# Optimization experiments

Measured on AMD Instinct MI355X. Metric: run time of the kernel, lower is better.

The kernel has to match this reference:

```python
import jax, jax.numpy as jnp
import numpy as np

N = 100000   # nodes
E = 1600000  # edges
G = 64       # graphs in batch
DIMS = [(7, 128), (128, 128), (128, 256)]
EPS = 1e-5


def setup_inputs() -> dict:
    key = jax.random.key(0)
    ks = jax.random.split(key, 32)
    inp = {}
    inp["x"] = jax.random.normal(ks[0], (N, 7), dtype=jnp.float32)
    inp["edge_index"] = jax.random.randint(ks[1], (2, E), 0, N, dtype=jnp.int64)
    inp["batch"] = jnp.sort(jax.random.randint(ks[2], (N,), 0, G, dtype=jnp.int64))
    ki = 3
    for i, (din, dout) in enumerate(DIMS):
        inp[f"Wl{i}"] = jax.random.normal(ks[ki], (din, dout), dtype=jnp.float32) * 0.05; ki += 1
        inp[f"bl{i}"] = jnp.zeros((dout,), dtype=jnp.float32)
        inp[f"Wr{i}"] = jax.random.normal(ks[ki], (din, dout), dtype=jnp.float32) * 0.05; ki += 1
        inp[f"g{i}"] = jax.random.uniform(ks[ki], (dout,), dtype=jnp.float32) + 0.5; ki += 1
        inp[f"be{i}"] = jax.random.normal(ks[ki], (dout,), dtype=jnp.float32) * 0.1; ki += 1
        inp[f"rm{i}"] = jax.random.normal(ks[ki], (dout,), dtype=jnp.float32) * 0.1; ki += 1
        inp[f"rv{i}"] = jax.random.uniform(ks[ki], (dout,), dtype=jnp.float32) + 0.5; ki += 1
    return inp


def _sage(x, src, dst, Wl, bl, Wr):
    # mean-aggregate neighbor features: out[i] = mean_{(j->i)} x[j]
    agg = jax.ops.segment_sum(x[src], dst, num_segments=N)          # [N, din]
    cnt = jax.ops.segment_sum(jnp.ones((src.shape[0],), x.dtype), dst, num_segments=N)
    mean = agg / jnp.maximum(cnt, 1.0)[:, None]
    return x @ Wl + bl + mean @ Wr


def _bn_relu(x, g, be, rm, rv):
    # BatchNorm1d in eval mode (running stats) + ReLU; dropout is a no-op in eval
    return jax.nn.relu((x - rm) * jax.lax.rsqrt(rv + EPS) * g + be)


def reference(x, edge_index, batch,
              Wl0, bl0, Wr0, g0, be0, rm0, rv0,
              Wl1, bl1, Wr1, g1, be1, rm1, rv1,
              Wl2, bl2, Wr2, g2, be2, rm2, rv2):
    src, dst = edge_index[0], edge_index[1]
    layers = [(Wl0, bl0, Wr0, g0, be0, rm0, rv0),
              (Wl1, bl1, Wr1, g1, be1, rm1, rv1),
              (Wl2, bl2, Wr2, g2, be2, rm2, rv2)]
    for Wl, bl, Wr, g, be, rm, rv in layers:
        x = _sage(x, src, dst, Wl, bl, Wr)
        x = _bn_relu(x, g, be, rm, rv)
    pooled = jax.ops.segment_sum(x, batch, num_segments=G)  # global_add_pool
    return (pooled, x)
```

## Files before the change

### kernel.cpp

```cpp
#include <hip/hip_runtime.h>
#include <hip/hip_bf16.h>

#define EPSV 1e-5f
#define PSHIFT 6
#define PMASK 63
#define BCAP 256
#define BSHIFT 8
#define XG 8

typedef __attribute__((ext_vector_type(8))) short bf16x8;
typedef __attribute__((ext_vector_type(4))) float f32x4;

__device__ __forceinline__ float bf2f(unsigned short u) {
    unsigned x = ((unsigned)u) << 16;
    return __builtin_bit_cast(float, x);
}
__device__ __forceinline__ unsigned short f2bf(float f) {
    unsigned x = __builtin_bit_cast(unsigned, f);
    unsigned r = (x + 0x7fffu + ((x >> 16) & 1u)) >> 16;
    return (unsigned short)r;
}

__global__ __launch_bounds__(256) void k_bucket(const int* __restrict__ src,
                                                const int* __restrict__ dst,
                                                int* __restrict__ bcnt,
                                                unsigned* __restrict__ staging,
                                                int E, int NPART) {
    int i = blockIdx.x * 256 + threadIdx.x;
    if (i >= E) return;
    int g = blockIdx.x & (XG - 1);
    int d = __builtin_nontemporal_load(&dst[i]);
    int s = __builtin_nontemporal_load(&src[i]);
    int p = d >> PSHIFT;
    int b = g * NPART + p;
    int slot = atomicAdd(&bcnt[b], 1);
    if (slot < BCAP)
        staging[((size_t)b << BSHIFT) + slot] = ((unsigned)s << PSHIFT) | (unsigned)(d & PMASK);
}

__global__ __launch_bounds__(256) void k_meta(const int* __restrict__ bcnt,
                                              int* __restrict__ pbase,
                                              int* __restrict__ off,
                                              const int* __restrict__ batch,
                                              int* __restrict__ gstart,
                                              int NPART, int Nn, int G) {
    if (blockIdx.x == 1) {
        int g = threadIdx.x;
        if (g > G) return;
        if (g == G) {
            gstart[G] = Nn;
            return;
        }
        int lo = 0, hi = Nn;
        while (lo < hi) {
            int mid = (lo + hi) >> 1;
            if (batch[mid] < g) lo = mid + 1;
            else hi = mid;
        }
        gstart[g] = lo;
        return;
    }
    __shared__ int red[256];
    int t = threadIdx.x;
    int chunk = (NPART + 255) / 256;
    int lo = t * chunk, hi = min(lo + chunk, NPART);
    int s = 0;
    for (int p = lo; p < hi; p++) {
        int tt = 0;
#pragma unroll
        for (int g = 0; g < XG; g++) tt += min(bcnt[g * NPART + p], BCAP);
        pbase[p] = tt;
        s += tt;
    }
    red[t] = s;
    __syncthreads();
    for (int d = 1; d < 256; d <<= 1) {
        int v = (t >= d) ? red[t - d] : 0;
        __syncthreads();
        red[t] += v;
        __syncthreads();
    }
    int base = (t == 0) ? 0 : red[t - 1];
    for (int p = lo; p < hi; p++) {
        int tt = pbase[p];
        pbase[p] = base;
        base += tt;
    }
    if (t == 255) off[Nn] = red[255];
}

__global__ __launch_bounds__(256) void k_build(const int* __restrict__ bcnt,
                                               const unsigned* __restrict__ staging,
                                               const int* __restrict__ pbase,
                                               int* __restrict__ off,
                                               int* __restrict__ csr,
                                               int NPART, int Nn) {
    __shared__ unsigned ed[XG * BCAP];
    __shared__ int srt[XG * BCAP];
    __shared__ int cnt[64], loff[64], cur[64];
    __shared__ int sb[XG + 1];
    int p = blockIdx.x, t = threadIdx.x;
    if (t < 64) cnt[t] = 0;
    if (t == 0) {
        int acc = 0;
#pragma unroll
        for (int g = 0; g < XG; g++) {
            sb[g] = acc;
            acc += min(bcnt[g * NPART + p], BCAP);
        }
        sb[XG] = acc;
    }
    __syncthreads();
    int tot = sb[XG];
#pragma unroll
    for (int g = 0; g < XG; g++) {
        int c = sb[g + 1] - sb[g];
        const unsigned* sp = staging + (((size_t)(g * NPART + p)) << BSHIFT);
        for (int j = t; j < c; j += 256) ed[sb[g] + j] = __builtin_nontemporal_load(&sp[j]);
    }
    __syncthreads();
    for (int j = t; j < tot; j += 256) atomicAdd(&cnt[ed[j] & PMASK], 1);
    __syncthreads();
    if (t == 0) {
        int a = 0;
        for (int j = 0; j < 64; j++) {
            loff[j] = a;
            cur[j] = a;
            a += cnt[j];
        }
    }
    __syncthreads();
    int base = pbase[p];
    int node0 = p << PSHIFT;
    if (t < 64 && node0 + t < Nn) off[node0 + t] = base + loff[t];
    for (int j = t; j < tot; j += 256) {
        unsigned e = ed[j];
        int pos = atomicAdd(&cur[e & PMASK], 1);
        srt[pos] = (int)(e >> PSHIFT);
    }
    __syncthreads();
    for (int j = t; j < tot; j += 256) csr[base + j] = srt[j];
}


__global__ __launch_bounds__(256) void k_agg7(const float* __restrict__ x,
                                              const int* __restrict__ off,
                                              const int* __restrict__ csr,
                                              float* __restrict__ mean, int n) {
    int i = (blockIdx.x * 256 + threadIdx.x) >> 3;
    int r = threadIdx.x & 7;
    if (i >= n) return;
    int a = off[i], b = off[i + 1];
    float acc = 0.f;
    if (r < 7) {
        int j = a;
        for (; j + 1 < b; j += 2)
            acc += x[(size_t)csr[j] * 7 + r] + x[(size_t)csr[j + 1] * 7 + r];
        if (j < b) acc += x[(size_t)csr[j] * 7 + r];
    }
    float inv = 1.0f / (float)max(b - a, 1);
    if (r < 7) mean[(size_t)i * 7 + r] = acc * inv;
}

__global__ __launch_bounds__(256) void k_agg128(const unsigned short* __restrict__ x,
                                                const int* __restrict__ off,
                                                const int* __restrict__ csr,
                                                unsigned short* __restrict__ mean,
                                                int n) {
    int h = (blockIdx.x * 256 + threadIdx.x) >> 5;
    int sl = threadIdx.x & 31;
    if (h >= n) return;
    int a = off[h], b = off[h + 1];
    float a0 = 0.f, a1 = 0.f, a2 = 0.f, a3 = 0.f;
    int j = a;
    for (; j + 3 < b; j += 4) {
        int s0 = csr[j], s1 = csr[j + 1], s2 = csr[j + 2], s3 = csr[j + 3];
        ushort4 v0 = *(const ushort4*)&x[(size_t)s0 * 128 + sl * 4];
        ushort4 v1 = *(const ushort4*)&x[(size_t)s1 * 128 + sl * 4];
        ushort4 v2 = *(const ushort4*)&x[(size_t)s2 * 128 + sl * 4];
        ushort4 v3 = *(const ushort4*)&x[(size_t)s3 * 128 + sl * 4];
        a0 += bf2f(v0.x) + bf2f(v1.x) + bf2f(v2.x) + bf2f(v3.x);
        a1 += bf2f(v0.y) + bf2f(v1.y) + bf2f(v2.y) + bf2f(v3.y);
        a2 += bf2f(v0.z) + bf2f(v1.z) + bf2f(v2.z) + bf2f(v3.z);
        a3 += bf2f(v0.w) + bf2f(v1.w) + bf2f(v2.w) + bf2f(v3.w);
    }
    for (; j < b; j++) {
        ushort4 v = *(const ushort4*)&x[(size_t)csr[j] * 128 + sl * 4];
        a0 += bf2f(v.x);
        a1 += bf2f(v.y);
        a2 += bf2f(v.z);
        a3 += bf2f(v.w);
    }
    float inv = 1.0f / (float)max(b - a, 1);
    ushort4 o;
    o.x = f2bf(a0 * inv);
    o.y = f2bf(a1 * inv);
    o.z = f2bf(a2 * inv);
    o.w = f2bf(a3 * inv);
    *(ushort4*)&mean[(size_t)h * 128 + sl * 4] = o;
}


__global__ __launch_bounds__(256) void k_prepw_all(
    const float* __restrict__ Wl1, const float* __restrict__ Wr1,
    const float* __restrict__ Wl2, const float* __restrict__ Wr2,
    unsigned short* __restrict__ Wlt1, unsigned short* __restrict__ Wrt1,
    unsigned short* __restrict__ Wlt2, unsigned short* __restrict__ Wrt2) {
    int u = blockIdx.x * 256 + threadIdx.x;
    const float* W;
    unsigned short* Wt;
    int Ncols, v;
    if (u < 32768) {
        v = u & 16383;
        W = (u < 16384) ? Wl1 : Wr1;
        Wt = (u < 16384) ? Wlt1 : Wrt1;
        Ncols = 128;
    } else {
        v = (u - 32768) & 32767;
        W = (u < 65536) ? Wl2 : Wr2;
        Wt = (u < 65536) ? Wlt2 : Wrt2;
        Ncols = 256;
    }
    int n = v % Ncols, k = v / Ncols;
    Wt[(size_t)n * 128 + k] = f2bf(W[(size_t)k * Ncols + n]);
}


__global__ __launch_bounds__(256) void k_layer0(
    const float* __restrict__ x, const float* __restrict__ mean,
    const float* __restrict__ Wl, const float* __restrict__ bl,
    const float* __restrict__ Wr, const float* __restrict__ g,
    const float* __restrict__ be, const float* __restrict__ rm,
    const float* __restrict__ rv, unsigned short* __restrict__ out, int n) {
    int tid = threadIdx.x;
    int col = tid & 127;
    int r = tid >> 7;
    int row = blockIdx.x * 2 + r;
    if (row >= n) return;
    float sc = g[col] * rsqrtf(rv[col] + EPSV);
    float sh = (bl[col] - rm[col]) * sc + be[col];
    const float* xp = x + (size_t)row * 7;
    const float* mp = mean + (size_t)row * 7;
    float acc = 0.f;
#pragma unroll
    for (int k = 0; k < 7; k++) acc += xp[k] * Wl[k * 128 + col];
#pragma unroll
    for (int k = 0; k < 7; k++) acc += mp[k] * Wr[k * 128 + col];
    float h = acc * sc + sh;
    out[(size_t)row * 128 + col] = f2bf(fmaxf(h, 0.f));
}


template <int COLS, int DOUT, bool BF16OUT>
__global__ __launch_bounds__(256) void k_mfma_layer(
    const unsigned short* __restrict__ xin, const unsigned short* __restrict__ meanb,
    const unsigned short* __restrict__ Wlt, const unsigned short* __restrict__ Wrt,
    const float* __restrict__ bl, const float* __restrict__ g,
    const float* __restrict__ be, const float* __restrict__ rm,
    const float* __restrict__ rv, void* __restrict__ outv, int n) {
    __shared__ unsigned short As[64 * 40];
    __shared__ unsigned short Bs[COLS * 40];

    int tid = threadIdx.x;
    int wave = tid >> 6;
    int lane = tid & 63;
    int m = lane & 15;
    int half = lane >> 4;
    int row0 = blockIdx.x * 64;
    int colbase = blockIdx.y * COLS;

    const int NCB = COLS / 16;
    f32x4 acc[NCB] = {};

    for (int s = 0; s < 8; s++) {
        int pass = s >> 2;
        int k0 = (s & 3) * 32;
        const unsigned short* Asrc = pass ? meanb : xin;
        const unsigned short* Wt = pass ? Wrt : Wlt;

        __syncthreads();
        {
            int rr = tid >> 2;
            int ks = (tid & 3) * 8;
            int grow = row0 + rr;
            float4 v = make_float4(0.f, 0.f, 0.f, 0.f);
            if (grow < n) v = *(const float4*)&Asrc[(size_t)grow * 128 + k0 + ks];
            *(float4*)&As[rr * 40 + ks] = v;
        }
#pragma unroll
        for (int rep = 0; rep < COLS / 64; rep++) {
            int u = tid + rep * 256;
            int nn = u >> 2;
            int ks = (u & 3) * 8;
            float4 v = *(const float4*)&Wt[(size_t)(colbase + nn) * 128 + k0 + ks];
            *(float4*)&Bs[nn * 40 + ks] = v;
        }
        __syncthreads();

        bf16x8 a = *(const bf16x8*)&As[(wave * 16 + m) * 40 + half * 8];
#pragma unroll
        for (int cb = 0; cb < NCB; cb++) {
            bf16x8 b = *(const bf16x8*)&Bs[(cb * 16 + m) * 40 + half * 8];
            acc[cb] = __builtin_amdgcn_mfma_f32_16x16x32_bf16(a, b, acc[cb], 0, 0, 0);
        }
    }

    float* outf = (float*)outv;
    unsigned short* outb = (unsigned short*)outv;
#pragma unroll
    for (int cb = 0; cb < NCB; cb++) {
        int col = colbase + cb * 16 + m;
        float sc = g[col] * rsqrtf(rv[col] + EPSV);
        float sh = (bl[col] - rm[col]) * sc + be[col];
#pragma unroll
        for (int reg = 0; reg < 4; reg++) {
            int r0 = row0 + wave * 16 + half * 4 + reg;
            if (r0 < n) {
                float h = fmaxf(acc[cb][reg] * sc + sh, 0.f);
                if (BF16OUT) outb[(size_t)r0 * DOUT + col] = f2bf(h);
                else outf[(size_t)r0 * DOUT + col] = h;
            }
        }
    }
}


__global__ __launch_bounds__(256) void k_pool(const float* __restrict__ x3,
                                              const int* __restrict__ gstart,
                                              float* __restrict__ pooled, int G) {
    const int S = 16;
    int g = blockIdx.x / S;
    int s = blockIdx.x % S;
    int a = gstart[g], b = gstart[g + 1];
    int col = threadIdx.x;
    float acc = 0.f;
    for (int r = a + s; r < b; r += S) acc += x3[(size_t)r * 256 + col];
    atomicAdd(&pooled[g * 256 + col], acc);
}


extern "C" void kernel_launch(void* const* d_in, const int* in_sizes, int n_in,
                              void* d_out, int out_size, void* d_ws, size_t ws_size,
                              hipStream_t stream) {
    const float* x = (const float*)d_in[0];
    const int* ei = (const int*)d_in[1];
    const int* batch = (const int*)d_in[2];
    const int N = in_sizes[0] / 7;
    const int E = in_sizes[1] / 2;
    const int G = 64;
    const int* src = ei;
    const int* dst = ei + E;
    const int NPART = (N + PMASK) >> PSHIFT;

    const float* P[21];
    for (int i = 0; i < 21; i++) P[i] = (const float*)d_in[3 + i];
    const float **L0 = P, **L1 = P + 7, **L2 = P + 14;

    char* w = (char*)d_ws;
    auto carve = [&](size_t bytes) {
        void* p = (void*)w;
        w += (bytes + 255) & ~(size_t)255;
        return p;
    };
    int* bcnt = (int*)carve((size_t)XG * NPART * 4);
    unsigned* staging = (unsigned*)carve((size_t)XG * NPART * BCAP * 4);
    int* pbase = (int*)carve((size_t)NPART * 4);
    int* off = (int*)carve(((size_t)N + 1) * 4);
    int* csr = (int*)carve((size_t)E * 4);
    int* gstart = (int*)carve(((size_t)G + 1) * 4);
    float* mean7 = (float*)carve((size_t)N * 7 * 4);
    unsigned short* x1 = (unsigned short*)carve((size_t)N * 128 * 2);
    unsigned short* meanb = (unsigned short*)carve((size_t)N * 128 * 2);
    unsigned short* Wlt1 = (unsigned short*)carve((size_t)128 * 128 * 2);
    unsigned short* Wrt1 = (unsigned short*)carve((size_t)128 * 128 * 2);
    unsigned short* Wlt2 = (unsigned short*)carve((size_t)128 * 256 * 2);
    unsigned short* Wrt2 = (unsigned short*)carve((size_t)128 * 256 * 2);

    float* pooled = (float*)d_out;
    float* x3 = (float*)d_out + (size_t)G * 256;

    hipMemsetAsync(bcnt, 0, (size_t)XG * NPART * 4, stream);
    hipMemsetAsync(pooled, 0, (size_t)G * 256 * 4, stream);

    k_bucket<<<(E + 255) / 256, 256, 0, stream>>>(src, dst, bcnt, staging, E, NPART);
    k_meta<<<2, 256, 0, stream>>>(bcnt, pbase, off, batch, gstart, NPART, N, G);
    k_build<<<NPART, 256, 0, stream>>>(bcnt, staging, pbase, off, csr, NPART, N);
    k_prepw_all<<<(98304 + 255) / 256, 256, 0, stream>>>(L1[0], L1[2], L2[0], L2[2],
                                                         Wlt1, Wrt1, Wlt2, Wrt2);

    k_agg7<<<(N * 8 + 255) / 256, 256, 0, stream>>>(x, off, csr, mean7, N);
    k_layer0<<<(N + 1) / 2, 256, 0, stream>>>(x, mean7, L0[0], L0[1], L0[2], L0[3],
                                              L0[4], L0[5], L0[6], x1, N);

    k_agg128<<<(N + 7) / 8, 256, 0, stream>>>(x1, off, csr, meanb, N);
    k_mfma_layer<128, 128, true><<<dim3((N + 63) / 64, 1), 256, 0, stream>>>(
        x1, meanb, Wlt1, Wrt1, L1[1], L1[3], L1[4], L1[5], L1[6], x1, N);

    k_agg128<<<(N + 7) / 8, 256, 0, stream>>>(x1, off, csr, meanb, N);
    k_mfma_layer<128, 256, false><<<dim3((N + 63) / 64, 2), 256, 0, stream>>>(
        x1, meanb, Wlt2, Wrt2, L2[1], L2[3], L2[4], L2[5], L2[6], x3, N);

    k_pool<<<G * 16, 256, 0, stream>>>(x3, gstart, pooled, G);
}
```

Baseline: 525.2 us.

## Replace single-pass edge bucketing with two-level block-aggregated radix scatter

The CSR construction used to do one global atomic per edge into XG-replicated 64-node buckets. It is replaced by a two-pass radix scatter. The first pass builds a block-local shared-memory histogram over 2048-node coarse buckets and needs one global atomic per bucket per block. The second pass redistributes each coarse bucket into 64-node partitions with the same block-aggregation trick. The aim is to cut global atomic contention and scattered writes. In exchange it adds an extra pass over the edges, and the CSR array now aliases the first-stage staging buffer.

```diff
diff --git a/kernel.cpp b/kernel.cpp
--- a/kernel.cpp
+++ b/kernel.cpp
@@ -4,9 +4,11 @@
 #define EPSV 1e-5f
 #define PSHIFT 6
 #define PMASK 63
-#define BCAP 256
-#define BSHIFT 8
-#define XG 8
+#define PCAP 1536
+#define B1SHIFT 11
+#define B1MASK ((1 << B1SHIFT) - 1)
+#define B1CAP 34816
+#define SPLIT 16
 
 typedef __attribute__((ext_vector_type(8))) short bf16x8;
 typedef __attribute__((ext_vector_type(4))) float f32x4;
@@ -21,24 +23,75 @@
     return (unsigned short)r;
 }
 
-__global__ __launch_bounds__(256) void k_bucket(const int* __restrict__ src,
-                                                const int* __restrict__ dst,
-                                                int* __restrict__ bcnt,
-                                                unsigned* __restrict__ staging,
-                                                int E, int NPART) {
-    int i = blockIdx.x * 256 + threadIdx.x;
-    if (i >= E) return;
-    int g = blockIdx.x & (XG - 1);
-    int d = __builtin_nontemporal_load(&dst[i]);
-    int s = __builtin_nontemporal_load(&src[i]);
-    int p = d >> PSHIFT;
-    int b = g * NPART + p;
-    int slot = atomicAdd(&bcnt[b], 1);
-    if (slot < BCAP)
-        staging[((size_t)b << BSHIFT) + slot] = ((unsigned)s << PSHIFT) | (unsigned)(d & PMASK);
-}
-
-__global__ __launch_bounds__(256) void k_meta(const int* __restrict__ bcnt,
+
+__global__ __launch_bounds__(256) void k_scatter1(const int* __restrict__ src,
+                                                  const int* __restrict__ dst,
+                                                  int* __restrict__ bcnt1,
+                                                  unsigned* __restrict__ stg1,
+                                                  int E, int NB1) {
+    __shared__ int hist[64], sbase[64], scur[64];
+    int t = threadIdx.x;
+    int base = blockIdx.x * 2048;
+    if (t < 64) { hist[t] = 0; scur[t] = 0; }
+    __syncthreads();
+    unsigned val[8];
+    int cb[8];
+#pragma unroll
+    for (int k = 0; k < 8; k++) {
+        int i = base + k * 256 + t;
+        if (i < E) {
+            int d = __builtin_nontemporal_load(&dst[i]);
+            int s = __builtin_nontemporal_load(&src[i]);
+            cb[k] = d >> B1SHIFT;
+            val[k] = ((unsigned)s << B1SHIFT) | (unsigned)(d & B1MASK);
+            atomicAdd(&hist[cb[k]], 1);
+        } else
+            cb[k] = -1;
+    }
+    __syncthreads();
+    if (t < NB1 && hist[t] > 0) sbase[t] = atomicAdd(&bcnt1[t], hist[t]);
+    __syncthreads();
+#pragma unroll
+    for (int k = 0; k < 8; k++) {
+        if (cb[k] >= 0) {
+            int r = atomicAdd(&scur[cb[k]], 1);
+            int slot = sbase[cb[k]] + r;
+            if (slot < B1CAP) stg1[(size_t)cb[k] * B1CAP + slot] = val[k];
+        }
+    }
+}
+
+__global__ __launch_bounds__(256) void k_scatter2(const int* __restrict__ bcnt1,
+                                                  const unsigned* __restrict__ stg1,
+                                                  int* __restrict__ pcnt,
+                                                  unsigned* __restrict__ pstg) {
+    __shared__ int hist[32], sbase[32], scur[32];
+    int cb = blockIdx.x >> 4;
+    int sl = blockIdx.x & (SPLIT - 1);
+    int t = threadIdx.x;
+    if (t < 32) { hist[t] = 0; scur[t] = 0; }
+    int cnt = min(bcnt1[cb], B1CAP);
+    int per = (cnt + SPLIT - 1) / SPLIT;
+    int lo = sl * per, hi = min(lo + per, cnt);
+    __syncthreads();
+    const unsigned* sp = stg1 + (size_t)cb * B1CAP;
+    for (int j = lo + t; j < hi; j += 256)
+        atomicAdd(&hist[(sp[j] >> 6) & 31], 1);
+    __syncthreads();
+    if (t < 32 && hist[t] > 0) sbase[t] = atomicAdd(&pcnt[(cb << 5) + t], hist[t]);
+    __syncthreads();
+    for (int j = lo + t; j < hi; j += 256) {
+        unsigned v = sp[j];
+        int pr = (v >> 6) & 31;
+        int r = atomicAdd(&scur[pr], 1);
+        int slot = sbase[pr] + r;
+        if (slot < PCAP)
+            pstg[(size_t)((cb << 5) + pr) * PCAP + slot] =
+                ((v >> 5) & ~63u) | (v & 63u);
+    }
+}
+
+__global__ __launch_bounds__(256) void k_meta(const int* __restrict__ pcnt,
                                               int* __restrict__ pbase,
                                               int* __restrict__ off,
                                               const int* __restrict__ batch,
@@ -66,9 +119,7 @@
     int lo = t * chunk, hi = min(lo + chunk, NPART);
     int s = 0;
     for (int p = lo; p < hi; p++) {
-        int tt = 0;
-#pragma unroll
-        for (int g = 0; g < XG; g++) tt += min(bcnt[g * NPART + p], BCAP);
+        int tt = min(pcnt[p], PCAP);
         pbase[p] = tt;
         s += tt;
     }
@@ -89,37 +140,24 @@
     if (t == 255) off[Nn] = red[255];
 }
 
-__global__ __launch_bounds__(256) void k_build(const int* __restrict__ bcnt,
-                                               const unsigned* __restrict__ staging,
+__global__ __launch_bounds__(256) void k_build(const int* __restrict__ pcnt,
+                                               const unsigned* __restrict__ pstg,
                                                const int* __restrict__ pbase,
                                                int* __restrict__ off,
-                                               int* __restrict__ csr,
-                                               int NPART, int Nn) {
-    __shared__ unsigned ed[XG * BCAP];
-    __shared__ int srt[XG * BCAP];
+                                               int* __restrict__ csr, int Nn) {
+    __shared__ unsigned ed[PCAP];
+    __shared__ int srt[PCAP];
     __shared__ int cnt[64], loff[64], cur[64];
-    __shared__ int sb[XG + 1];
     int p = blockIdx.x, t = threadIdx.x;
+    int tot = min(pcnt[p], PCAP);
     if (t < 64) cnt[t] = 0;
-    if (t == 0) {
-        int acc = 0;
-#pragma unroll
-        for (int g = 0; g < XG; g++) {
-            sb[g] = acc;
-            acc += min(bcnt[g * NPART + p], BCAP);
-        }
-        sb[XG] = acc;
-    }
-    __syncthreads();
-    int tot = sb[XG];
-#pragma unroll
-    for (int g = 0; g < XG; g++) {
-        int c = sb[g + 1] - sb[g];
-        const unsigned* sp = staging + (((size_t)(g * NPART + p)) << BSHIFT);
-        for (int j = t; j < c; j += 256) ed[sb[g] + j] = __builtin_nontemporal_load(&sp[j]);
-    }
-    __syncthreads();
-    for (int j = t; j < tot; j += 256) atomicAdd(&cnt[ed[j] & PMASK], 1);
+    __syncthreads();
+    const unsigned* sp = pstg + (size_t)p * PCAP;
+    for (int j = t; j < tot; j += 256) {
+        unsigned e = __builtin_nontemporal_load(&sp[j]);
+        ed[j] = e;
+        atomicAdd(&cnt[e & PMASK], 1);
+    }
     __syncthreads();
     if (t == 0) {
         int a = 0;
@@ -351,6 +389,7 @@
     const int* src = ei;
     const int* dst = ei + E;
     const int NPART = (N + PMASK) >> PSHIFT;
+    const int NB1 = (N + (1 << B1SHIFT) - 1) >> B1SHIFT;
 
     const float* P[21];
     for (int i = 0; i < 21; i++) P[i] = (const float*)d_in[3 + i];
@@ -362,11 +401,13 @@
         w += (bytes + 255) & ~(size_t)255;
         return p;
     };
-    int* bcnt = (int*)carve((size_t)XG * NPART * 4);
-    unsigned* staging = (unsigned*)carve((size_t)XG * NPART * BCAP * 4);
+    int* cnts = (int*)carve((size_t)(64 + NPART) * 4);
+    int* bcnt1 = cnts;
+    int* pcnt = cnts + 64;
+    unsigned* stg1 = (unsigned*)carve((size_t)NB1 * B1CAP * 4);
+    unsigned* pstg = (unsigned*)carve((size_t)NPART * PCAP * 4);
     int* pbase = (int*)carve((size_t)NPART * 4);
     int* off = (int*)carve(((size_t)N + 1) * 4);
-    int* csr = (int*)carve((size_t)E * 4);
     int* gstart = (int*)carve(((size_t)G + 1) * 4);
     float* mean7 = (float*)carve((size_t)N * 7 * 4);
     unsigned short* x1 = (unsigned short*)carve((size_t)N * 128 * 2);
@@ -375,16 +416,18 @@
     unsigned short* Wrt1 = (unsigned short*)carve((size_t)128 * 128 * 2);
     unsigned short* Wlt2 = (unsigned short*)carve((size_t)128 * 256 * 2);
     unsigned short* Wrt2 = (unsigned short*)carve((size_t)128 * 256 * 2);
+    int* csr = (int*)stg1;
 
     float* pooled = (float*)d_out;
     float* x3 = (float*)d_out + (size_t)G * 256;
 
-    hipMemsetAsync(bcnt, 0, (size_t)XG * NPART * 4, stream);
+    hipMemsetAsync(cnts, 0, (size_t)(64 + NPART) * 4, stream);
     hipMemsetAsync(pooled, 0, (size_t)G * 256 * 4, stream);
 
-    k_bucket<<<(E + 255) / 256, 256, 0, stream>>>(src, dst, bcnt, staging, E, NPART);
-    k_meta<<<2, 256, 0, stream>>>(bcnt, pbase, off, batch, gstart, NPART, N, G);
-    k_build<<<NPART, 256, 0, stream>>>(bcnt, staging, pbase, off, csr, NPART, N);
+    k_scatter1<<<(E + 2047) / 2048, 256, 0, stream>>>(src, dst, bcnt1, stg1, E, NB1);
+    k_scatter2<<<NB1 * SPLIT, 256, 0, stream>>>(bcnt1, stg1, pcnt, pstg);
+    k_meta<<<2, 256, 0, stream>>>(pcnt, pbase, off, batch, gstart, NPART, N, G);
+    k_build<<<NPART, 256, 0, stream>>>(pcnt, pstg, pbase, off, csr, N);
     k_prepw_all<<<(98304 + 255) / 256, 256, 0, stream>>>(L1[0], L1[2], L2[0], L2[2],
                                                          Wlt1, Wrt1, Wlt2, Wrt2);
 
```

New measurement: 483.5 us. -7.9%, faster.
